# Optimization experiments

Hardware: AMD Instinct MI355X
Metric: run time of the kernel (lower is better)

The kernel has to match this reference:

```python
import jax, jax.numpy as jnp
import numpy as np

H = 64      # hidden_size
I = 46      # input_size
NC = 8      # num_classes


def setup_inputs() -> dict:
    key = jax.random.key(0)
    ks = jax.random.split(key, 12)
    B, T = 2048, 256
    s = 1.0 / np.sqrt(H)  # torch default init scale for LSTM/Linear

    def u(k, shape):
        return jax.random.uniform(k, shape, jnp.float32, -s, s)

    x = jax.random.normal(ks[0], (B, T, I), dtype=jnp.float32)
    return {
        "x": x,
        # forward-direction LSTM params (gate order i,f,g,o as in torch)
        "Wih_f": u(ks[1], (4 * H, I)),
        "Whh_f": u(ks[2], (4 * H, H)),
        "bih_f": u(ks[3], (4 * H,)),
        "bhh_f": u(ks[4], (4 * H,)),
        # backward-direction LSTM params
        "Wih_b": u(ks[5], (4 * H, I)),
        "Whh_b": u(ks[6], (4 * H, H)),
        "bih_b": u(ks[7], (4 * H,)),
        "bhh_b": u(ks[8], (4 * H,)),
        # final linear
        "fcW": u(ks[9], (NC, 2 * H)),
        "fcb": u(ks[10], (NC,)),
    }


def _lstm_scan(x_tbi, Wih, Whh, bih, bhh):
    """Unidirectional LSTM over time-major input (T,B,I). Returns all hidden states (T,B,H)."""
    T, B, _ = x_tbi.shape
    h_dim = Whh.shape[1]
    # precompute input projections for all timesteps: (T,B,4H)
    xp = jnp.einsum('tbi,gi->tbg', x_tbi, Wih) + bih + bhh

    def step(carry, xp_t):
        h, c = carry
        z = xp_t + h @ Whh.T  # (B,4H)
        i, f, g, o = jnp.split(z, 4, axis=-1)
        i = jax.nn.sigmoid(i)
        f = jax.nn.sigmoid(f)
        g = jnp.tanh(g)
        o = jax.nn.sigmoid(o)
        c = f * c + i * g
        h = o * jnp.tanh(c)
        return (h, c), h

    h0 = jnp.zeros((B, h_dim), x_tbi.dtype)
    _, hs = jax.lax.scan(step, (h0, h0), xp)
    return hs


def reference(x, Wih_f, Whh_f, bih_f, bhh_f, Wih_b, Whh_b, bih_b, bhh_b, fcW, fcb):
    # x: (B,T,I) -> time-major (T,B,I), matching x.transpose(0,1)
    xt = jnp.transpose(x, (1, 0, 2))
    hf = _lstm_scan(xt, Wih_f, Whh_f, bih_f, bhh_f)            # (T,B,H) forward dir
    hb = _lstm_scan(xt[::-1], Wih_b, Whh_b, bih_b, bhh_b)      # scan over reversed seq
    # r_out[-1] = concat(forward hidden at t=T-1, backward hidden at t=T-1)
    # backward hidden at original t=T-1 is the FIRST step of the reversed scan
    last = jnp.concatenate([hf[-1], hb[0]], axis=-1)            # (B, 2H)
    logits = last @ fcW.T + fcb                                 # (B, NC)
    return jax.nn.softmax(logits, axis=1)
```

## Files before the change

kernel.cpp:

```cpp
#include <hip/hip_runtime.h>
#include <math.h>

#define TT   256
#define HH   64
#define INw  46
#define NCLS 8
#define BB   8
#define CH   4
#define NCH  (TT / CH)
#define B2   8
#define XS   80
#define XCHS 20

typedef __attribute__((ext_vector_type(8))) short  short8v;
typedef __attribute__((ext_vector_type(4))) float  float4v;

__device__ __forceinline__ float frcp(float x) { return __builtin_amdgcn_rcpf(x); }
__device__ __forceinline__ float sigmoid_f(float x) { return frcp(1.f + __expf(-x)); }
__device__ __forceinline__ float tanh_f(float x) {
    float a = fabsf(x);
    float e = __expf(-2.f * a);
    float r = (1.f - e) * frcp(1.f + e);
    return x >= 0.f ? r : -r;
}
__device__ __forceinline__ float dot4(float4 w, float4 a, float acc) {
    acc = fmaf(w.x, a.x, acc);
    acc = fmaf(w.y, a.y, acc);
    acc = fmaf(w.z, a.z, acc);
    acc = fmaf(w.w, a.w, acc);
    return acc;
}

__device__ __forceinline__ unsigned short f2bf(float f) {
    unsigned int u = __float_as_uint(f);
    unsigned int r = u + 0x7FFFu + ((u >> 16) & 1u);
    return (unsigned short)(r >> 16);
}
__device__ __forceinline__ float bf2f(unsigned short h) {
    return __uint_as_float(((unsigned int)h) << 16);
}
__device__ __forceinline__ void split8(const float v[8], short8v& hi, short8v& lo) {
#pragma unroll
    for (int e = 0; e < 8; ++e) {
        unsigned short h = f2bf(v[e]);
        hi[e] = (short)h;
        lo[e] = (short)f2bf(v[e] - bf2f(h));
    }
}

#define MFMA16(A,B,C) __builtin_amdgcn_mfma_f32_16x16x32_bf16((A),(B),(C),0,0,0)

__global__ __launch_bounds__(1024, 1) void lstm_fwd_mfma(
    const float* __restrict__ x,
    const float* __restrict__ Wih,
    const float* __restrict__ Whh,
    const float* __restrict__ bih,
    const float* __restrict__ bhh,
    float* __restrict__ hf_out)
{
    __shared__ float zx[2][CH][4][HH][8];
    __shared__ short x_hi[CH][BB][XS];
    __shared__ short x_lo[CH][BB][XS];
    __shared__ short h_hi[2][BB][XS];
    __shared__ short h_lo[2][BB][XS];
    __shared__ float xch[HH * XCHS];

    const int j    = threadIdx.x;
    const int w    = j >> 6;
    const int l    = j & 63;
    const int g    = l >> 4;
    const int c16  = l & 15;
    const int b0   = blockIdx.x * BB;
    const int wl   = w & 3;
    const int u    = 16 * wl + c16;
    const int r0p  = ((g & 1) * 4) ^ (u & 4);
    const bool isP  = (w >= 8);
    const bool isGO = (w >= 4 && w < 8);
    const bool isIF = (w < 4);
    const int  pg   = (w >= 12) ? 1 : 0;
    const bool hi2  = (g & 2) != 0;
    const int  row0 = 4 * (g & 1) + 2 * (g >> 1);
    const int  xofs = 8 * (g & 1) + 4 * (g >> 1);

    short8v wf[4][2];
    float bias2[2] = {0.f, 0.f};
    if (!isP) {
        const int cb0 = isGO ? 128 : 0;
#pragma unroll
        for (int tq = 0; tq < 2; ++tq) {
            const int n = cb0 + 64 * tq + u;
            bias2[tq] = bih[n] + bhh[n];
#pragma unroll
            for (int s2 = 0; s2 < 2; ++s2) {
                float vh[8];
#pragma unroll
                for (int e = 0; e < 8; ++e)
                    vh[e] = Whh[n * HH + 32 * s2 + 8 * g + e];
                split8(vh, wf[tq][s2], wf[2 + tq][s2]);
            }
        }
    } else {
#pragma unroll
        for (int qq = 0; qq < 2; ++qq) {
            const int n = 64 * (2 * pg + qq) + u;
#pragma unroll
            for (int s2 = 0; s2 < 2; ++s2) {
                float vi[8];
#pragma unroll
                for (int e = 0; e < 8; ++e) {
                    const int k = 32 * s2 + 8 * g + e;
                    const float tval = Wih[n * INw + ((k < INw) ? k : 0)];
                    vi[e] = (k < INw) ? tval : 0.f;
                }
                split8(vi, wf[qq][s2], wf[2 + qq][s2]);
            }
        }
    }

    {
        short* hh0 = &h_hi[0][0][0];
        short* hl0 = &h_lo[0][0][0];
        for (int idx = j; idx < 2 * BB * XS; idx += 1024) {
            hh0[idx] = 0;
            hl0[idx] = 0;
        }
        short* xh0 = &x_hi[0][0][0];
        short* xl0 = &x_lo[0][0][0];
        for (int idx = j; idx < CH * BB * XS; idx += 1024) {
            xh0[idx] = 0;
            xl0[idx] = 0;
        }
    }
    __syncthreads();

    for (int e = j; e < BB * CH * INw; e += 1024) {
        const int r   = e / (CH * INw);
        const int rem = e - r * (CH * INw);
        const int tt  = rem / INw;
        const int k   = rem - tt * INw;
        const float v = x[((size_t)(b0 + r) * TT + tt) * INw + k];
        const unsigned short hh = f2bf(v);
        x_hi[tt][r][k] = (short)hh;
        x_lo[tt][r][k] = (short)f2bf(v - bf2f(hh));
    }
    __syncthreads();

    auto zx_burst = [&](int tau, int nbuf) {
        const int trel = 2 * tau + (c16 >> 3);
        const int rr   = c16 & 7;
        const short* ph = &x_hi[trel][rr][0] + 8 * g;
        const short* pl = &x_lo[trel][rr][0] + 8 * g;
        const short8v axh0 = *(const short8v*)(ph);
        const short8v axh1 = *(const short8v*)(ph + 32);
        const short8v axl0 = *(const short8v*)(pl);
        const short8v axl1 = *(const short8v*)(pl + 32);
        const int tout = 2 * tau + (g >> 1);
#pragma unroll
        for (int qq = 0; qq < 2; ++qq) {
            const int q = 2 * pg + qq;
            float4v C = {0.f, 0.f, 0.f, 0.f};
            C = MFMA16(axh0, wf[qq][0], C);
            C = MFMA16(axh1, wf[qq][1], C);
            C = MFMA16(axh0, wf[2 + qq][0], C);
            C = MFMA16(axh1, wf[2 + qq][1], C);
            C = MFMA16(axl0, wf[qq][0], C);
            C = MFMA16(axl1, wf[qq][1], C);
            *(float4v*)&zx[nbuf][tout][q][u][r0p] = C;
        }
    };

    size_t st_gof[3]; int st_lds[3]; bool st_ok[3];
#pragma unroll
    for (int it = 0; it < 3; ++it) {
        const int e  = (j - 512) + 512 * it;
        const bool ok = (e >= 0) && (e < BB * CH * INw);
        const int ec = ok ? e : 0;
        const int r   = ec / (CH * INw);
        const int rem = ec - r * (CH * INw);
        const int tt  = rem / INw;
        const int k   = rem - tt * INw;
        st_ok[it]  = ok;
        st_gof[it] = ((size_t)(b0 + r) * TT + tt) * INw + k;
        st_lds[it] = (tt * BB + r) * XS + k;
    }
    short* xsh = &x_hi[0][0][0];
    short* xsl = &x_lo[0][0][0];

    float xhold[3];
    if (isP) {
        zx_burst(0, 0);
        zx_burst(1, 0);
#pragma unroll
        for (int it = 0; it < 3; ++it)
            if (st_ok[it]) xhold[it] = x[st_gof[it] + (size_t)(CH * INw)];
    }

    float cst2[2]  = {0.f, 0.f};
    float hnew2[2] = {0.f, 0.f};
    __syncthreads();

    for (int c = 0; c < NCH; ++c) {
        const int cb = c & 1, nb = cb ^ 1;
#pragma unroll
        for (int s = 0; s < CH; ++s) {
            const int t = c * CH + s;
            float iv0, fv0, iv1, fv1;
            if (!isP) {
                const short* hrh = &h_hi[(t + 1) & 1][0][0];
                const short* hrl = &h_lo[(t + 1) & 1][0][0];
                const int ro = (c16 & 7) * XS;
                const short8v ahh0 = *(const short8v*)(hrh + ro + 8 * g);
                const short8v ahh1 = *(const short8v*)(hrh + ro + 32 + 8 * g);
                const short8v ahl0 = *(const short8v*)(hrl + ro + 8 * g);
                const short8v ahl1 = *(const short8v*)(hrl + ro + 32 + 8 * g);
                const int q0 = isGO ? 2 : 0;
                float4v C0 = *(const float4v*)&zx[cb][s][q0][u][r0p];
                float4v C1 = *(const float4v*)&zx[cb][s][q0 + 1][u][r0p];
                float4v D0 = {0.f, 0.f, 0.f, 0.f};
                float4v D1 = {0.f, 0.f, 0.f, 0.f};
                __builtin_amdgcn_s_setprio(1);
                C0 = MFMA16(ahh0, wf[0][0], C0);
                C1 = MFMA16(ahh0, wf[1][0], C1);
                D0 = MFMA16(ahl0, wf[0][0], D0);
                D1 = MFMA16(ahl0, wf[1][0], D1);
                C0 = MFMA16(ahh1, wf[0][1], C0);
                C1 = MFMA16(ahh1, wf[1][1], C1);
                D0 = MFMA16(ahl1, wf[0][1], D0);
                D1 = MFMA16(ahl1, wf[1][1], D1);
                D0 = MFMA16(ahh0, wf[2][0], D0);
                D1 = MFMA16(ahh0, wf[3][0], D1);
                D0 = MFMA16(ahh1, wf[2][1], D0);
                D1 = MFMA16(ahh1, wf[3][1], D1);
                __builtin_amdgcn_s_setprio(0);
                C0 += D0;
                C1 += D1;
                const float c0a = hi2 ? C0[2] : C0[0];
                const float c1a = hi2 ? C1[2] : C1[0];
                const float c0b = hi2 ? C0[3] : C0[1];
                const float c1b = hi2 ? C1[3] : C1[1];
                if (isGO) {
                    float4v A;
                    A[0] = tanh_f(c0a + bias2[0]);
                    A[1] = sigmoid_f(c1a + bias2[1]);
                    A[2] = tanh_f(c0b + bias2[0]);
                    A[3] = sigmoid_f(c1b + bias2[1]);
                    *(float4v*)&xch[u * XCHS + xofs] = A;
                } else {
                    iv0 = sigmoid_f(c0a + bias2[0]);
                    fv0 = sigmoid_f(c1a + bias2[1]);
                    iv1 = sigmoid_f(c0b + bias2[0]);
                    fv1 = sigmoid_f(c1b + bias2[1]);
                }
            } else {
                if (s == 1 && c + 1 < NCH) {
                    zx_burst(0, nb);
                } else if (s == 3 && c + 2 < NCH) {
                    const size_t cofs = (size_t)(c + 2) * (CH * INw);
#pragma unroll
                    for (int it = 0; it < 3; ++it)
                        if (st_ok[it]) xhold[it] = x[st_gof[it] + cofs];
                }
            }
            __syncthreads();
            if (isIF) {
                const float4v A = *(const float4v*)&xch[u * XCHS + xofs];
                cst2[0] = fmaf(fv0, cst2[0], iv0 * A[0]);
                hnew2[0] = A[1] * tanh_f(cst2[0]);
                cst2[1] = fmaf(fv1, cst2[1], iv1 * A[2]);
                hnew2[1] = A[3] * tanh_f(cst2[1]);
                short* hwh = &h_hi[t & 1][0][0] + row0 * XS + u;
                short* hwl = &h_lo[t & 1][0][0] + row0 * XS + u;
                const unsigned short h0h = f2bf(hnew2[0]);
                hwh[0]  = (short)h0h;
                hwl[0]  = (short)f2bf(hnew2[0] - bf2f(h0h));
                const unsigned short h1h = f2bf(hnew2[1]);
                hwh[XS] = (short)h1h;
                hwl[XS] = (short)f2bf(hnew2[1] - bf2f(h1h));
            } else if (isP) {
                if (s == 0 && c + 1 < NCH) {
#pragma unroll
                    for (int it = 0; it < 3; ++it) {
                        if (st_ok[it]) {
                            const unsigned short hh = f2bf(xhold[it]);
                            xsh[st_lds[it]] = (short)hh;
                            xsl[st_lds[it]] = (short)f2bf(xhold[it] - bf2f(hh));
                        }
                    }
                } else if (s == 2 && c + 1 < NCH) {
                    zx_burst(1, nb);
                }
            }
            __syncthreads();
        }
    }

    if (isIF) {
        hf_out[(size_t)(b0 + row0)     * HH + u] = hnew2[0];
        hf_out[(size_t)(b0 + row0 + 1) * HH + u] = hnew2[1];
    }
}

__global__ __launch_bounds__(256) void lstm_bwd_fc(
    const float* __restrict__ x,
    const float* __restrict__ Wih,
    const float* __restrict__ bih,
    const float* __restrict__ bhh,
    const float* __restrict__ fcW,
    const float* __restrict__ fcb,
    const float* __restrict__ hf,
    float* __restrict__ out)
{
    __shared__ float xl[B2][48];
    __shared__ float act[B2][256];
    __shared__ float hbl[B2][HH];

    const int j  = threadIdx.x;
    const int b0 = blockIdx.x * B2;

    for (int e = j; e < B2 * INw; e += 256) {
        int b = e / INw, i = e - b * INw;
        xl[b][i] = x[((size_t)(b0 + b) * TT + (TT - 1)) * INw + i];
    }
    if (j < B2) { xl[j][46] = 0.f; xl[j][47] = 0.f; }
    __syncthreads();

    float4 wih4[12];
#pragma unroll
    for (int ii = 0; ii < 11; ++ii)
        wih4[ii] = make_float4(Wih[j*INw + 4*ii + 0], Wih[j*INw + 4*ii + 1],
                               Wih[j*INw + 4*ii + 2], Wih[j*INw + 4*ii + 3]);
    wih4[11] = make_float4(Wih[j*INw + 44], Wih[j*INw + 45], 0.f, 0.f);
    const float bias = bih[j] + bhh[j];
    const bool  gate_is_tanh = ((j >> 6) == 2);

#pragma unroll
    for (int b = 0; b < B2; ++b) {
        float a = bias;
#pragma unroll
        for (int ii = 0; ii < 12; ++ii) {
            float4 xv = *(const float4*)&xl[b][4*ii];
            a = dot4(wih4[ii], xv, a);
        }
        act[b][j] = gate_is_tanh ? tanh_f(a) : sigmoid_f(a);
    }
    __syncthreads();

    for (int q = j; q < B2 * HH; q += 256) {
        int b = q >> 6, ll = q & 63;
        float ig = act[b][ll];
        float gg = act[b][128 + ll];
        float og = act[b][192 + ll];
        hbl[b][ll] = og * tanh_f(ig * gg);
    }
    __syncthreads();

    if (j < B2 * NCLS) {
        int b = j >> 3, n = j & 7;
        float a = fcb[n];
        const float* hfr = hf + (size_t)(b0 + b) * HH;
#pragma unroll
        for (int ll = 0; ll < HH; ++ll) {
            a = fmaf(fcW[n * 2 * HH + ll],      hfr[ll],    a);
            a = fmaf(fcW[n * 2 * HH + HH + ll], hbl[b][ll], a);
        }
        float m = a;
        m = fmaxf(m, __shfl_xor(m, 1, 8));
        m = fmaxf(m, __shfl_xor(m, 2, 8));
        m = fmaxf(m, __shfl_xor(m, 4, 8));
        float e = __expf(a - m);
        float s = e;
        s += __shfl_xor(s, 1, 8);
        s += __shfl_xor(s, 2, 8);
        s += __shfl_xor(s, 4, 8);
        out[(size_t)(b0 + b) * NCLS + n] = e / s;
    }
}

extern "C" void kernel_launch(void* const* d_in, const int* in_sizes, int n_in,
                              void* d_out, int out_size, void* d_ws, size_t ws_size,
                              hipStream_t stream) {
    const float* x     = (const float*)d_in[0];
    const float* Wih_f = (const float*)d_in[1];
    const float* Whh_f = (const float*)d_in[2];
    const float* bih_f = (const float*)d_in[3];
    const float* bhh_f = (const float*)d_in[4];
    const float* Wih_b = (const float*)d_in[5];
    const float* bih_b = (const float*)d_in[7];
    const float* bhh_b = (const float*)d_in[8];
    const float* fcW   = (const float*)d_in[9];
    const float* fcb   = (const float*)d_in[10];
    float* out = (float*)d_out;
    float* hf  = (float*)d_ws;

    hipLaunchKernelGGL(lstm_fwd_mfma, dim3(2048 / BB), dim3(1024), 0, stream,
                       x, Wih_f, Whh_f, bih_f, bhh_f, hf);
    hipLaunchKernelGGL(lstm_bwd_fc, dim3(2048 / B2), dim3(256), 0, stream,
                       x, Wih_b, bih_b, bhh_b, fcW, fcb, hf, out);
}
```

Baseline: 215.3 us.

## Merge gate warps so each compute warp evaluates all four LSTM gates

The 4 IF warps and 4 GO warps are merged into 4 compute warps that each hold all four gate weight slices and do the full recurrent MFMA and cell update themselves. This removes the LDS exchange buffer and one __syncthreads per timestep. The block shrinks from 1024 to 768 threads with launch bounds (768,3), so more blocks can be resident. In exchange each compute warp issues twice as many MFMAs on the serial critical path and needs more registers for weights.

```diff
diff --git a/kernel.cpp b/kernel.cpp
--- a/kernel.cpp
+++ b/kernel.cpp
@@ -10,7 +10,6 @@
 #define NCH  (TT / CH)
 #define B2   8
 #define XS   80
-#define XCHS 20
 
 typedef __attribute__((ext_vector_type(8))) short  short8v;
 typedef __attribute__((ext_vector_type(4))) float  float4v;
@@ -50,7 +49,7 @@
 
 #define MFMA16(A,B,C) __builtin_amdgcn_mfma_f32_16x16x32_bf16((A),(B),(C),0,0,0)
 
-__global__ __launch_bounds__(1024, 1) void lstm_fwd_mfma(
+__global__ __launch_bounds__(768, 3) void lstm_fwd_mfma(
     const float* __restrict__ x,
     const float* __restrict__ Wih,
     const float* __restrict__ Whh,
@@ -63,7 +62,6 @@
     __shared__ short x_lo[CH][BB][XS];
     __shared__ short h_hi[2][BB][XS];
     __shared__ short h_lo[2][BB][XS];
-    __shared__ float xch[HH * XCHS];
 
     const int j    = threadIdx.x;
     const int w    = j >> 6;
@@ -74,29 +72,26 @@
     const int wl   = w & 3;
     const int u    = 16 * wl + c16;
     const int r0p  = ((g & 1) * 4) ^ (u & 4);
-    const bool isP  = (w >= 8);
-    const bool isGO = (w >= 4 && w < 8);
-    const bool isIF = (w < 4);
-    const int  pg   = (w >= 12) ? 1 : 0;
+    const bool isC  = (w < 4);
+    const bool isP  = !isC;
+    const int  pg   = (w >= 8) ? 1 : 0;
     const bool hi2  = (g & 2) != 0;
     const int  row0 = 4 * (g & 1) + 2 * (g >> 1);
-    const int  xofs = 8 * (g & 1) + 4 * (g >> 1);
-
-    short8v wf[4][2];
-    float bias2[2] = {0.f, 0.f};
-    if (!isP) {
-        const int cb0 = isGO ? 128 : 0;
-#pragma unroll
-        for (int tq = 0; tq < 2; ++tq) {
-            const int n = cb0 + 64 * tq + u;
-            bias2[tq] = bih[n] + bhh[n];
+
+    short8v wf[8][2];
+    float bias4[4] = {0.f, 0.f, 0.f, 0.f};
+    if (isC) {
+#pragma unroll
+        for (int q = 0; q < 4; ++q) {
+            const int n = 64 * q + u;
+            bias4[q] = bih[n] + bhh[n];
 #pragma unroll
             for (int s2 = 0; s2 < 2; ++s2) {
                 float vh[8];
 #pragma unroll
                 for (int e = 0; e < 8; ++e)
                     vh[e] = Whh[n * HH + 32 * s2 + 8 * g + e];
-                split8(vh, wf[tq][s2], wf[2 + tq][s2]);
+                split8(vh, wf[q][s2], wf[4 + q][s2]);
             }
         }
     } else {
@@ -120,20 +115,20 @@
     {
         short* hh0 = &h_hi[0][0][0];
         short* hl0 = &h_lo[0][0][0];
-        for (int idx = j; idx < 2 * BB * XS; idx += 1024) {
+        for (int idx = j; idx < 2 * BB * XS; idx += 768) {
             hh0[idx] = 0;
             hl0[idx] = 0;
         }
         short* xh0 = &x_hi[0][0][0];
         short* xl0 = &x_lo[0][0][0];
-        for (int idx = j; idx < CH * BB * XS; idx += 1024) {
+        for (int idx = j; idx < CH * BB * XS; idx += 768) {
             xh0[idx] = 0;
             xl0[idx] = 0;
         }
     }
     __syncthreads();
 
-    for (int e = j; e < BB * CH * INw; e += 1024) {
+    for (int e = j; e < BB * CH * INw; e += 768) {
         const int r   = e / (CH * INw);
         const int rem = e - r * (CH * INw);
         const int tt  = rem / INw;
@@ -172,7 +167,7 @@
     size_t st_gof[3]; int st_lds[3]; bool st_ok[3];
 #pragma unroll
     for (int it = 0; it < 3; ++it) {
-        const int e  = (j - 512) + 512 * it;
+        const int e  = (j - 256) + 512 * it;
         const bool ok = (e >= 0) && (e < BB * CH * INw);
         const int ec = ok ? e : 0;
         const int r   = ec / (CH * INw);
@@ -204,8 +199,7 @@
 #pragma unroll
         for (int s = 0; s < CH; ++s) {
             const int t = c * CH + s;
-            float iv0, fv0, iv1, fv1;
-            if (!isP) {
+            if (isC) {
                 const short* hrh = &h_hi[(t + 1) & 1][0][0];
                 const short* hrl = &h_lo[(t + 1) & 1][0][0];
                 const int ro = (c16 & 7) * XS;
@@ -213,9 +207,11 @@
                 const short8v ahh1 = *(const short8v*)(hrh + ro + 32 + 8 * g);
                 const short8v ahl0 = *(const short8v*)(hrl + ro + 8 * g);
                 const short8v ahl1 = *(const short8v*)(hrl + ro + 32 + 8 * g);
-                const int q0 = isGO ? 2 : 0;
-                float4v C0 = *(const float4v*)&zx[cb][s][q0][u][r0p];
-                float4v C1 = *(const float4v*)&zx[cb][s][q0 + 1][u][r0p];
+                const float* zr = &zx[cb][s][0][u][r0p];
+                float4v C0 = *(const float4v*)(zr);
+                float4v C1 = *(const float4v*)(zr + 512);
+                float4v C2 = *(const float4v*)(zr + 1024);
+                float4v C3 = *(const float4v*)(zr + 1536);
                 float4v D0 = {0.f, 0.f, 0.f, 0.f};
                 float4v D1 = {0.f, 0.f, 0.f, 0.f};
                 __builtin_amdgcn_s_setprio(1);
@@ -227,47 +223,39 @@
                 C1 = MFMA16(ahh1, wf[1][1], C1);
                 D0 = MFMA16(ahl1, wf[0][1], D0);
                 D1 = MFMA16(ahl1, wf[1][1], D1);
-                D0 = MFMA16(ahh0, wf[2][0], D0);
-                D1 = MFMA16(ahh0, wf[3][0], D1);
-                D0 = MFMA16(ahh1, wf[2][1], D0);
-                D1 = MFMA16(ahh1, wf[3][1], D1);
-                __builtin_amdgcn_s_setprio(0);
+                D0 = MFMA16(ahh0, wf[4][0], D0);
+                D1 = MFMA16(ahh0, wf[5][0], D1);
+                D0 = MFMA16(ahh1, wf[4][1], D0);
+                D1 = MFMA16(ahh1, wf[5][1], D1);
                 C0 += D0;
                 C1 += D1;
-                const float c0a = hi2 ? C0[2] : C0[0];
-                const float c1a = hi2 ? C1[2] : C1[0];
-                const float c0b = hi2 ? C0[3] : C0[1];
-                const float c1b = hi2 ? C1[3] : C1[1];
-                if (isGO) {
-                    float4v A;
-                    A[0] = tanh_f(c0a + bias2[0]);
-                    A[1] = sigmoid_f(c1a + bias2[1]);
-                    A[2] = tanh_f(c0b + bias2[0]);
-                    A[3] = sigmoid_f(c1b + bias2[1]);
-                    *(float4v*)&xch[u * XCHS + xofs] = A;
-                } else {
-                    iv0 = sigmoid_f(c0a + bias2[0]);
-                    fv0 = sigmoid_f(c1a + bias2[1]);
-                    iv1 = sigmoid_f(c0b + bias2[0]);
-                    fv1 = sigmoid_f(c1b + bias2[1]);
+                float4v E0 = {0.f, 0.f, 0.f, 0.f};
+                float4v E1 = {0.f, 0.f, 0.f, 0.f};
+                C2 = MFMA16(ahh0, wf[2][0], C2);
+                C3 = MFMA16(ahh0, wf[3][0], C3);
+                E0 = MFMA16(ahl0, wf[2][0], E0);
+                E1 = MFMA16(ahl0, wf[3][0], E1);
+                C2 = MFMA16(ahh1, wf[2][1], C2);
+                C3 = MFMA16(ahh1, wf[3][1], C3);
+                E0 = MFMA16(ahl1, wf[2][1], E0);
+                E1 = MFMA16(ahl1, wf[3][1], E1);
+                E0 = MFMA16(ahh0, wf[6][0], E0);
+                E1 = MFMA16(ahh0, wf[7][0], E1);
+                E0 = MFMA16(ahh1, wf[6][1], E0);
+                E1 = MFMA16(ahh1, wf[7][1], E1);
+                __builtin_amdgcn_s_setprio(0);
+                C2 += E0;
+                C3 += E1;
+                const int ri = hi2 ? 2 : 0;
+#pragma unroll
+                for (int rr = 0; rr < 2; ++rr) {
+                    const float iv = sigmoid_f(C0[ri + rr] + bias4[0]);
+                    const float fv = sigmoid_f(C1[ri + rr] + bias4[1]);
+                    const float gv = tanh_f   (C2[ri + rr] + bias4[2]);
+                    const float ov = sigmoid_f(C3[ri + rr] + bias4[3]);
+                    cst2[rr]  = fmaf(fv, cst2[rr], iv * gv);
+                    hnew2[rr] = ov * tanh_f(cst2[rr]);
                 }
-            } else {
-                if (s == 1 && c + 1 < NCH) {
-                    zx_burst(0, nb);
-                } else if (s == 3 && c + 2 < NCH) {
-                    const size_t cofs = (size_t)(c + 2) * (CH * INw);
-#pragma unroll
-                    for (int it = 0; it < 3; ++it)
-                        if (st_ok[it]) xhold[it] = x[st_gof[it] + cofs];
-                }
-            }
-            __syncthreads();
-            if (isIF) {
-                const float4v A = *(const float4v*)&xch[u * XCHS + xofs];
-                cst2[0] = fmaf(fv0, cst2[0], iv0 * A[0]);
-                hnew2[0] = A[1] * tanh_f(cst2[0]);
-                cst2[1] = fmaf(fv1, cst2[1], iv1 * A[2]);
-                hnew2[1] = A[3] * tanh_f(cst2[1]);
                 short* hwh = &h_hi[t & 1][0][0] + row0 * XS + u;
                 short* hwl = &h_lo[t & 1][0][0] + row0 * XS + u;
                 const unsigned short h0h = f2bf(hnew2[0]);
@@ -276,7 +264,7 @@
                 const unsigned short h1h = f2bf(hnew2[1]);
                 hwh[XS] = (short)h1h;
                 hwl[XS] = (short)f2bf(hnew2[1] - bf2f(h1h));
-            } else if (isP) {
+            } else {
                 if (s == 0 && c + 1 < NCH) {
 #pragma unroll
                     for (int it = 0; it < 3; ++it) {
@@ -286,15 +274,22 @@
                             xsl[st_lds[it]] = (short)f2bf(xhold[it] - bf2f(hh));
                         }
                     }
+                } else if (s == 1 && c + 1 < NCH) {
+                    zx_burst(0, nb);
                 } else if (s == 2 && c + 1 < NCH) {
                     zx_burst(1, nb);
+                } else if (s == 3 && c + 2 < NCH) {
+                    const size_t cofs = (size_t)(c + 2) * (CH * INw);
+#pragma unroll
+                    for (int it = 0; it < 3; ++it)
+                        if (st_ok[it]) xhold[it] = x[st_gof[it] + cofs];
                 }
             }
             __syncthreads();
         }
     }
 
-    if (isIF) {
+    if (isC) {
         hf_out[(size_t)(b0 + row0)     * HH + u] = hnew2[0];
         hf_out[(size_t)(b0 + row0 + 1) * HH + u] = hnew2[1];
     }
@@ -392,7 +387,7 @@
     float* out = (float*)d_out;
     float* hf  = (float*)d_ws;
 
-    hipLaunchKernelGGL(lstm_fwd_mfma, dim3(2048 / BB), dim3(1024), 0, stream,
+    hipLaunchKernelGGL(lstm_fwd_mfma, dim3(2048 / BB), dim3(768), 0, stream,
                        x, Wih_f, Whh_f, bih_f, bhh_f, hf);
     hipLaunchKernelGGL(lstm_bwd_fc, dim3(2048 / B2), dim3(256), 0, stream,
                        x, Wih_b, bih_b, bhh_b, fcW, fcb, hf, out);
```

Result: faster. 175.0 us (median of 2 runs) (-18.7%).
